# Kernel tuning notes

Measured on AMD Instinct MI355X. Metric: run time of the kernel, lower is better.

Reference implementation:

```python
import jax, jax.numpy as jnp
import numpy as np

N_NODES = 50000
N_EDGES = 800000
IN_FEATS = 128
HIDDEN = 128
NUM_CLASSES = 47


def setup_inputs() -> dict:
    key = jax.random.key(0)
    k1, k2, k3, k4 = jax.random.split(key, 4)
    features = jax.random.normal(k1, (N_NODES, IN_FEATS), dtype=jnp.float32)
    edge_index = jax.random.randint(k2, (2, N_EDGES), 0, N_NODES, dtype=jnp.int32)
    # Glorot-style init for weights, zeros for bias (DGL GraphConv defaults)
    W1 = jax.random.normal(k3, (IN_FEATS, HIDDEN), dtype=jnp.float32) * (1.0 / np.sqrt(IN_FEATS))
    b1 = jnp.zeros((HIDDEN,), dtype=jnp.float32)
    W2 = jax.random.normal(k4, (HIDDEN, NUM_CLASSES), dtype=jnp.float32) * (1.0 / np.sqrt(HIDDEN))
    b2 = jnp.zeros((NUM_CLASSES,), dtype=jnp.float32)
    return {"features": features, "edge_index": edge_index,
            "W1": W1, "b1": b1, "W2": W2, "b2": b2}


def _graph_conv(x, W, b, src, dst, norm_src, norm_dst, n_nodes):
    # DGL GraphConv, norm='both': D_dst^{-1/2} A D_src^{-1/2} (X W) + b
    h = (x * norm_src[:, None]) @ W            # transform before aggregation
    agg = jax.ops.segment_sum(h[src], dst, num_segments=n_nodes)
    return agg * norm_dst[:, None] + b


def reference(features, edge_index, W1, b1, W2, b2):
    src, dst = edge_index[0], edge_index[1]
    n = features.shape[0]
    ones = jnp.ones((src.shape[0],), dtype=features.dtype)
    deg_out = jax.ops.segment_sum(ones, src, num_segments=n)
    deg_in = jax.ops.segment_sum(ones, dst, num_segments=n)
    norm_src = jax.lax.rsqrt(jnp.clip(deg_out, 1.0))   # d_out^{-1/2}, clamp >= 1
    norm_dst = jax.lax.rsqrt(jnp.clip(deg_in, 1.0))    # d_in^{-1/2}, clamp >= 1

    h = _graph_conv(features, W1, b1, src, dst, norm_src, norm_dst, n)
    h = jax.nn.relu(h)
    out = _graph_conv(h, W2, b2, src, dst, norm_src, norm_dst, n)
    return out
```

## Files before the change

kernel.cpp:

```cpp
#include <hip/hip_runtime.h>
#include <hip/hip_fp16.h>

#define N_NODES 50000
#define N_EDGES 800000
#define IN_F 128
#define HID 128
#define NCLS 47
#define H2S 48
#define W2C 64
#define NCH 196
#define NB 128
#define CHUNK 6250
#define PDW 12500
#define HHALF 6250
#define FQ 3125
#define NHIST 512
#define G1ROWS 256
#define G2ROWS 128


typedef _Float16 f16x8 __attribute__((ext_vector_type(8)));
typedef float f32x4 __attribute__((ext_vector_type(4)));

struct __align__(8)  h2x2 { __half2 a, b; };
struct __align__(16) h2x4 { __half2 a, b, c, d; };

__global__ __launch_bounds__(512) void hist_kernel(const int* __restrict__ ei,
                                                   unsigned int* __restrict__ Pdst,
                                                   unsigned int* __restrict__ Psrc,
                                                   const float* __restrict__ W1,
                                                   const float* __restrict__ W2,
                                                   __half* __restrict__ W1Th,
                                                   __half* __restrict__ W1Tl,
                                                   __half* __restrict__ W2Th,
                                                   __half* __restrict__ W2Tl) {
    __shared__ unsigned int h[HHALF];
    const int t = threadIdx.x;
    const int job = blockIdx.x;
    if (job >= NHIST) {
        if (job == NHIST) {
            for (int i2 = t; i2 < W2C * HID; i2 += 512) {
                int cc = i2 >> 7, k = i2 & 127;
                float w = (cc < NCLS) ? W2[k * NCLS + cc] : 0.f;
                __half hv = __float2half_rn(w);
                W2Th[i2] = hv;
                W2Tl[i2] = __float2half_rn(w - __half2float(hv));
            }
        } else {
            for (int i2 = t; i2 < IN_F * HID; i2 += 512) {
                int cc = i2 >> 7, k = i2 & 127;
                float w = W1[k * HID + cc];
                __half hv = __float2half_rn(w);
                W1Th[i2] = hv;
                W1Tl[i2] = __float2half_rn(w - __half2float(hv));
            }
        }
        return;
    }
    const bool is_src = job >= NHIST / 2;
    const int half = (job >> 7) & 1;
    const int chunk = job & (NB - 1);
    const int* ids = is_src ? ei : ei + N_EDGES;
    uint2* h2 = (uint2*)h;
    for (int j = t; j < HHALF / 2; j += 512) h2[j] = make_uint2(0u, 0u);
    __syncthreads();
    const int e0 = chunk * CHUNK;
    const int lo = half * HHALF;
    const int2* e2p = (const int2*)(ids + e0);
    for (int k = t; k < CHUNK / 2; k += 512) {
        int2 v2 = e2p[k];
        int r0 = (v2.x >> 2) - lo;
        if ((unsigned)r0 < HHALF) atomicAdd(&h[r0], 1u << ((v2.x & 3) * 8));
        int r1 = (v2.y >> 2) - lo;
        if ((unsigned)r1 < HHALF) atomicAdd(&h[r1], 1u << ((v2.y & 3) * 8));
    }
    __syncthreads();
    unsigned int* P = (is_src ? Psrc : Pdst) + (size_t)chunk * PDW + lo;
    uint2* P2 = (uint2*)P;
    for (int j = t; j < HHALF / 2; j += 512) P2[j] = h2[j];
}

__global__ __launch_bounds__(256) void reduce_kernel(unsigned int* __restrict__ Pdst,
                                                     const unsigned int* __restrict__ Psrc,
                                                     int* __restrict__ cnt_in,
                                                     float* __restrict__ norm_src,
                                                     float* __restrict__ norm_dst,
                                                     int* __restrict__ chunk_sums) {
    __shared__ int sm[256];
    const int t = threadIdx.x;
    const int j = blockIdx.x * 256 + t;
    int tot = 0;
    if (j < PDW) {
        unsigned int run = 0;
#pragma unroll 8
        for (int b = 0; b < NB; ++b) {
            unsigned int v = Pdst[(size_t)b * PDW + j];
            Pdst[(size_t)b * PDW + j] = run;
            run += v;
        }
        int n0 = run & 0xff, n1 = (run >> 8) & 0xff;
        int n2 = (run >> 16) & 0xff, n3 = (run >> 24) & 0xff;
        *(int4*)&cnt_in[4 * j] = make_int4(n0, n1, n2, n3);
        *(float4*)&norm_dst[4 * j] = make_float4(
            rsqrtf(fmaxf((float)n0, 1.0f)), rsqrtf(fmaxf((float)n1, 1.0f)),
            rsqrtf(fmaxf((float)n2, 1.0f)), rsqrtf(fmaxf((float)n3, 1.0f)));
        tot = n0 + n1 + n2 + n3;
        unsigned int rs = 0;
#pragma unroll 8
        for (int b = 0; b < NB; ++b) rs += Psrc[(size_t)b * PDW + j];
        int s0 = rs & 0xff, s1 = (rs >> 8) & 0xff;
        int s2 = (rs >> 16) & 0xff, s3 = (rs >> 24) & 0xff;
        *(float4*)&norm_src[4 * j] = make_float4(
            rsqrtf(fmaxf((float)s0, 1.0f)), rsqrtf(fmaxf((float)s1, 1.0f)),
            rsqrtf(fmaxf((float)s2, 1.0f)), rsqrtf(fmaxf((float)s3, 1.0f)));
    }
    sm[t] = tot;
    __syncthreads();
    const int g = t & 63;
    for (int off = 32; off > 0; off >>= 1) {
        if (g < off) sm[t] += sm[t + off];
        __syncthreads();
    }
    if (g == 0) chunk_sums[blockIdx.x * 4 + (t >> 6)] = sm[t];
}

__global__ __launch_bounds__(256) void scan3_kernel(const int* __restrict__ cnt_in,
                                                    const int* __restrict__ chunk_sums,
                                                    int* __restrict__ offsets) {
    __shared__ int sm[256];
    const int t = threadIdx.x;
    int v = (t < NCH) ? chunk_sums[t] : 0;
    sm[t] = v;
    __syncthreads();
    for (int off = 1; off < 256; off <<= 1) {
        int u = (t >= off) ? sm[t - off] : 0;
        __syncthreads();
        sm[t] += u;
        __syncthreads();
    }
    const int basev = (blockIdx.x == 0) ? 0 : sm[blockIdx.x - 1];
    __syncthreads();
    const int idx = blockIdx.x * 256 + t;
    int c = (idx < N_NODES) ? cnt_in[idx] : 0;
    sm[t] = c;
    __syncthreads();
    for (int off = 1; off < 256; off <<= 1) {
        int u = (t >= off) ? sm[t - off] : 0;
        __syncthreads();
        sm[t] += u;
        __syncthreads();
    }
    if (idx < N_NODES) offsets[idx] = basev + sm[t] - c;
    if (blockIdx.x == 0 && t == 0) offsets[N_NODES] = N_EDGES;
}

__global__ __launch_bounds__(512) void fill_gemm1_kernel(const int* __restrict__ src,
        const int* __restrict__ dst, const int* __restrict__ offsets,
        const unsigned int* __restrict__ Pdst, int* __restrict__ csr_src,
        const float* __restrict__ X, const __half* __restrict__ W1Th,
        const __half* __restrict__ W1Tl, __half* __restrict__ H1h) {
    __shared__ __align__(16) unsigned int cur[FQ];
    const int t = threadIdx.x;
    if (blockIdx.x < 4 * NB) {
        const int quarter = blockIdx.x >> 7;
        const int chunk = blockIdx.x & (NB - 1);
        for (int j = t; j < FQ; j += 512) cur[j] = 0u;
        __syncthreads();
        const unsigned int* base = Pdst + (size_t)chunk * PDW;
        const int e0 = chunk * CHUNK;
        const int lo = quarter * FQ;
        const int2* d2p = (const int2*)(dst + e0);
        const int2* s2p = (const int2*)(src + e0);
        for (int k = t; k < CHUNK / 2; k += 512) {
            int2 d2 = d2p[k];
            int2 s2 = s2p[k];
            int r0 = (d2.x >> 2) - lo;
            if ((unsigned)r0 < FQ) {
                const int sh = (d2.x & 3) * 8;
                unsigned int old = atomicAdd(&cur[r0], 1u << sh);
                unsigned int rank = (old >> sh) & 0xffu;
                unsigned int bh = (base[d2.x >> 2] >> sh) & 0xffu;
                csr_src[offsets[d2.x] + (int)bh + (int)rank] = s2.x;
            }
            int r1 = (d2.y >> 2) - lo;
            if ((unsigned)r1 < FQ) {
                const int sh = (d2.y & 3) * 8;
                unsigned int old = atomicAdd(&cur[r1], 1u << sh);
                unsigned int rank = (old >> sh) & 0xffu;
                unsigned int bh = (base[d2.y >> 2] >> sh) & 0xffu;
                csr_src[offsets[d2.y] + (int)bh + (int)rank] = s2.y;
            }
        }
    } else {
        const int lane = t & 63;
        const int wv = t >> 6;
        const int r16 = lane & 15;
        const int kg = lane >> 4;
        const int row0 = (blockIdx.x - 4 * NB) * G1ROWS + wv * 32;
        f32x4 acc[2][8] = {};
#pragma unroll
        for (int s = 0; s < 4; ++s) {
            const int k0 = 32 * s + 8 * kg;
            f16x8 ah[2], al[2];
#pragma unroll
            for (int rt = 0; rt < 2; ++rt) {
                int row = row0 + rt * 16 + r16;
                int rc = row < N_NODES ? row : N_NODES - 1;
                const float4 x0 = *(const float4*)&X[(size_t)rc * IN_F + k0];
                const float4 x1 = *(const float4*)&X[(size_t)rc * IN_F + k0 + 4];
                const float xv[8] = {x0.x, x0.y, x0.z, x0.w,
                                     x1.x, x1.y, x1.z, x1.w};
#pragma unroll
                for (int j = 0; j < 8; ++j) {
                    _Float16 hv = (_Float16)xv[j];
                    ah[rt][j] = hv;
                    al[rt][j] = (_Float16)(xv[j] - (float)hv);
                }
            }
#pragma unroll
            for (int tt = 0; tt < 8; ++tt) {
                const f16x8 bh = *(const f16x8*)&W1Th[(16 * tt + r16) * IN_F + k0];
                const f16x8 bl = *(const f16x8*)&W1Tl[(16 * tt + r16) * IN_F + k0];
#pragma unroll
                for (int rt = 0; rt < 2; ++rt) {
                    acc[rt][tt] = __builtin_amdgcn_mfma_f32_16x16x32_f16(
                        ah[rt], bh, acc[rt][tt], 0, 0, 0);
                    acc[rt][tt] = __builtin_amdgcn_mfma_f32_16x16x32_f16(
                        al[rt], bh, acc[rt][tt], 0, 0, 0);
                    acc[rt][tt] = __builtin_amdgcn_mfma_f32_16x16x32_f16(
                        ah[rt], bl, acc[rt][tt], 0, 0, 0);
                }
            }
        }
#pragma unroll
        for (int rt = 0; rt < 2; ++rt)
#pragma unroll
            for (int j = 0; j < 4; ++j) {
                const int row = row0 + rt * 16 + 4 * kg + j;
                if (row < N_NODES) {
#pragma unroll
                    for (int tt = 0; tt < 8; ++tt)
                        H1h[(size_t)row * HID + 16 * tt + r16] =
                            __float2half_rn(acc[rt][tt][j]);
                }
            }
    }
}

__global__ __launch_bounds__(256) void gather1_kernel(const __half* __restrict__ H1h,
        const int* __restrict__ offsets, const int* __restrict__ csr_src,
        const float* __restrict__ b1, const float* __restrict__ norm_src,
        const float* __restrict__ norm_dst, __half* __restrict__ Hrelu16) {
    const int lane = threadIdx.x & 63;
    const int q = lane >> 4;
    const int fl = lane & 15;
    const int row = blockIdx.x * 4 + (threadIdx.x >> 6);
    const int beg = offsets[row], end = offsets[row + 1];
    float a0 = 0.f, a1 = 0.f, a2 = 0.f, a3 = 0.f;
    float a4 = 0.f, a5 = 0.f, a6 = 0.f, a7 = 0.f;
    for (int base = beg; base < end; base += 64) {
        int idx = 0;
        float nsv = 0.f;
        if (base + lane < end) {
            idx = csr_src[base + lane];
            nsv = norm_src[idx];
        }
        const int cnt = min(end - base, 64);
        for (int j = 0; j < cnt; j += 16) {
            int e0 = j + q, e1 = j + 4 + q, e2 = j + 8 + q, e3 = j + 12 + q;
            int s0 = __shfl(idx, e0);  float n0 = __shfl(nsv, e0);
            int s1 = __shfl(idx, e1);  float n1 = __shfl(nsv, e1);
            int s2 = __shfl(idx, e2);  float n2 = __shfl(nsv, e2);
            int s3 = __shfl(idx, e3);  float n3 = __shfl(nsv, e3);
            h2x4 v0 = *(const h2x4*)&H1h[(size_t)s0 * HID + 8 * fl];
            h2x4 v1 = *(const h2x4*)&H1h[(size_t)s1 * HID + 8 * fl];
            h2x4 v2 = *(const h2x4*)&H1h[(size_t)s2 * HID + 8 * fl];
            h2x4 v3 = *(const h2x4*)&H1h[(size_t)s3 * HID + 8 * fl];
            float2 f;
            f = __half22float2(v0.a); a0 = fmaf(f.x, n0, a0); a1 = fmaf(f.y, n0, a1);
            f = __half22float2(v0.b); a2 = fmaf(f.x, n0, a2); a3 = fmaf(f.y, n0, a3);
            f = __half22float2(v0.c); a4 = fmaf(f.x, n0, a4); a5 = fmaf(f.y, n0, a5);
            f = __half22float2(v0.d); a6 = fmaf(f.x, n0, a6); a7 = fmaf(f.y, n0, a7);
            f = __half22float2(v1.a); a0 = fmaf(f.x, n1, a0); a1 = fmaf(f.y, n1, a1);
            f = __half22float2(v1.b); a2 = fmaf(f.x, n1, a2); a3 = fmaf(f.y, n1, a3);
            f = __half22float2(v1.c); a4 = fmaf(f.x, n1, a4); a5 = fmaf(f.y, n1, a5);
            f = __half22float2(v1.d); a6 = fmaf(f.x, n1, a6); a7 = fmaf(f.y, n1, a7);
            f = __half22float2(v2.a); a0 = fmaf(f.x, n2, a0); a1 = fmaf(f.y, n2, a1);
            f = __half22float2(v2.b); a2 = fmaf(f.x, n2, a2); a3 = fmaf(f.y, n2, a3);
            f = __half22float2(v2.c); a4 = fmaf(f.x, n2, a4); a5 = fmaf(f.y, n2, a5);
            f = __half22float2(v2.d); a6 = fmaf(f.x, n2, a6); a7 = fmaf(f.y, n2, a7);
            f = __half22float2(v3.a); a0 = fmaf(f.x, n3, a0); a1 = fmaf(f.y, n3, a1);
            f = __half22float2(v3.b); a2 = fmaf(f.x, n3, a2); a3 = fmaf(f.y, n3, a3);
            f = __half22float2(v3.c); a4 = fmaf(f.x, n3, a4); a5 = fmaf(f.y, n3, a5);
            f = __half22float2(v3.d); a6 = fmaf(f.x, n3, a6); a7 = fmaf(f.y, n3, a7);
        }
    }
    a0 += __shfl_xor(a0, 16); a1 += __shfl_xor(a1, 16);
    a2 += __shfl_xor(a2, 16); a3 += __shfl_xor(a3, 16);
    a4 += __shfl_xor(a4, 16); a5 += __shfl_xor(a5, 16);
    a6 += __shfl_xor(a6, 16); a7 += __shfl_xor(a7, 16);
    a0 += __shfl_xor(a0, 32); a1 += __shfl_xor(a1, 32);
    a2 += __shfl_xor(a2, 32); a3 += __shfl_xor(a3, 32);
    a4 += __shfl_xor(a4, 32); a5 += __shfl_xor(a5, 32);
    a6 += __shfl_xor(a6, 32); a7 += __shfl_xor(a7, 32);
    if (lane < 16) {
        float nd = norm_dst[row], ns = norm_src[row];
        float4 bA = *(const float4*)&b1[8 * fl];
        float4 bB = *(const float4*)&b1[8 * fl + 4];
        float o0 = fmaxf(fmaf(a0, nd, bA.x), 0.f) * ns;
        float o1 = fmaxf(fmaf(a1, nd, bA.y), 0.f) * ns;
        float o2 = fmaxf(fmaf(a2, nd, bA.z), 0.f) * ns;
        float o3 = fmaxf(fmaf(a3, nd, bA.w), 0.f) * ns;
        float o4 = fmaxf(fmaf(a4, nd, bB.x), 0.f) * ns;
        float o5 = fmaxf(fmaf(a5, nd, bB.y), 0.f) * ns;
        float o6 = fmaxf(fmaf(a6, nd, bB.z), 0.f) * ns;
        float o7 = fmaxf(fmaf(a7, nd, bB.w), 0.f) * ns;
        h2x4 p = {__floats2half2_rn(o0, o1), __floats2half2_rn(o2, o3),
                  __floats2half2_rn(o4, o5), __floats2half2_rn(o6, o7)};
        *(h2x4*)&Hrelu16[(size_t)row * HID + 8 * fl] = p;
    }
}

__global__ __launch_bounds__(256) void gemm2_kernel(const __half* __restrict__ Hrelu16,
                                                    const __half* __restrict__ W2Th,
                                                    const __half* __restrict__ W2Tl,
                                                    __half* __restrict__ H2h) {
    const int lane = threadIdx.x & 63;
    const int wv = threadIdx.x >> 6;
    const int r16 = lane & 15;
    const int kg = lane >> 4;
    const int row0 = blockIdx.x * G2ROWS + wv * 32;
    f32x4 acc[2][3] = {};
#pragma unroll
    for (int s = 0; s < 4; ++s) {
        const int k0 = 32 * s + 8 * kg;
        f16x8 a[2];
#pragma unroll
        for (int rt = 0; rt < 2; ++rt) {
            int row = row0 + rt * 16 + r16;
            int rc = row < N_NODES ? row : N_NODES - 1;
            a[rt] = *(const f16x8*)&Hrelu16[(size_t)rc * HID + k0];
        }
#pragma unroll
        for (int tt = 0; tt < 3; ++tt) {
            const f16x8 bh = *(const f16x8*)&W2Th[(16 * tt + r16) * HID + k0];
            const f16x8 bl = *(const f16x8*)&W2Tl[(16 * tt + r16) * HID + k0];
#pragma unroll
            for (int rt = 0; rt < 2; ++rt) {
                acc[rt][tt] = __builtin_amdgcn_mfma_f32_16x16x32_f16(
                    a[rt], bh, acc[rt][tt], 0, 0, 0);
                acc[rt][tt] = __builtin_amdgcn_mfma_f32_16x16x32_f16(
                    a[rt], bl, acc[rt][tt], 0, 0, 0);
            }
        }
    }
#pragma unroll
    for (int rt = 0; rt < 2; ++rt)
#pragma unroll
        for (int j = 0; j < 4; ++j) {
            const int row = row0 + rt * 16 + 4 * kg + j;
            if (row < N_NODES) {
#pragma unroll
                for (int tt = 0; tt < 3; ++tt)
                    H2h[(size_t)row * H2S + 16 * tt + r16] =
                        __float2half_rn(acc[rt][tt][j]);
            }
        }
}

__global__ __launch_bounds__(256) void gather2_kernel(const __half* __restrict__ H2h,
        const int* __restrict__ offsets, const int* __restrict__ csr_src,
        const float* __restrict__ b2, const float* __restrict__ norm_dst,
        float* __restrict__ out) {
    const int lane = threadIdx.x & 63;
    const int row = blockIdx.x * 4 + (threadIdx.x >> 6);
    const int beg = offsets[row], end = offsets[row + 1];
    const int cl = min(lane, H2S - 1);
    float acc = 0.f;
    for (int base = beg; base < end; base += 64) {
        int idx = 0;
        float wv = 0.f;
        if (base + lane < end) {
            idx = csr_src[base + lane];
            wv = 1.f;
        }
        const int cnt = min(end - base, 64);
        for (int j = 0; j < cnt; j += 4) {
            int s0 = __shfl(idx, j);     float w0 = __shfl(wv, j);
            int s1 = __shfl(idx, j + 1); float w1 = __shfl(wv, j + 1);
            int s2 = __shfl(idx, j + 2); float w2 = __shfl(wv, j + 2);
            int s3 = __shfl(idx, j + 3); float w3 = __shfl(wv, j + 3);
            float f0 = __half2float(H2h[(size_t)s0 * H2S + cl]);
            float f1 = __half2float(H2h[(size_t)s1 * H2S + cl]);
            float f2 = __half2float(H2h[(size_t)s2 * H2S + cl]);
            float f3 = __half2float(H2h[(size_t)s3 * H2S + cl]);
            acc = fmaf(f0, w0, acc);
            acc = fmaf(f1, w1, acc);
            acc = fmaf(f2, w2, acc);
            acc = fmaf(f3, w3, acc);
        }
    }
    if (lane < NCLS) out[(size_t)row * NCLS + lane] = acc * norm_dst[row] + b2[lane];
}

extern "C" void kernel_launch(void* const* d_in, const int* in_sizes, int n_in,
                              void* d_out, int out_size, void* d_ws, size_t ws_size,
                              hipStream_t stream) {
    const float* X  = (const float*)d_in[0];
    const int*   ei = (const int*)d_in[1];
    const float* W1 = (const float*)d_in[2];
    const float* b1 = (const float*)d_in[3];
    const float* W2 = (const float*)d_in[4];
    const float* b2 = (const float*)d_in[5];
    float* out = (float*)d_out;

    const int* src = ei;
    const int* dst = ei + N_EDGES;

    char* w = (char*)d_ws;
    auto alloc = [&](size_t bytes) {
        char* p = w;
        w += (bytes + 255) & ~(size_t)255;
        return p;
    };
    float*  norm_src   = (float*)alloc(N_NODES * 4);
    float*  norm_dst   = (float*)alloc(N_NODES * 4);
    int*    cnt_in     = (int*)alloc(N_NODES * 4);
    int*    offsets    = (int*)alloc((N_NODES + 1) * 4);
    int*    csr_src    = (int*)alloc((size_t)N_EDGES * 4);
    int*    chunk_sums = (int*)alloc(NCH * 4);
    __half* W1Th       = (__half*)alloc((size_t)IN_F * HID * 2);
    __half* W1Tl       = (__half*)alloc((size_t)IN_F * HID * 2);
    __half* W2Th       = (__half*)alloc((size_t)W2C * HID * 2);
    __half* W2Tl       = (__half*)alloc((size_t)W2C * HID * 2);
    __half* H1h        = (__half*)alloc((size_t)N_NODES * HID * 2);
    __half* Hrelu16    = (__half*)alloc((size_t)N_NODES * HID * 2);
    __half* H2h        = (__half*)alloc((size_t)N_NODES * H2S * 2);
    unsigned int* Pdst = (unsigned int*)alloc((size_t)NB * PDW * 4);
    unsigned int* Psrc = (unsigned int*)alloc((size_t)NB * PDW * 4);

    const int g1_blocks = (N_NODES + G1ROWS - 1) / G1ROWS;
    const int g2_blocks = (N_NODES + G2ROWS - 1) / G2ROWS;
    hist_kernel<<<NHIST + 2, 512, 0, stream>>>(ei, Pdst, Psrc, W1, W2,
                                               W1Th, W1Tl, W2Th, W2Tl);
    reduce_kernel<<<(PDW + 255) / 256, 256, 0, stream>>>(Pdst, Psrc, cnt_in,
                                                         norm_src, norm_dst, chunk_sums);
    scan3_kernel<<<NCH, 256, 0, stream>>>(cnt_in, chunk_sums, offsets);
    fill_gemm1_kernel<<<4 * NB + g1_blocks, 512, 0, stream>>>(src, dst, offsets,
                                                              Pdst, csr_src,
                                                              X, W1Th, W1Tl, H1h);
    gather1_kernel<<<N_NODES / 4, 256, 0, stream>>>(H1h, offsets, csr_src, b1,
                                                    norm_src, norm_dst, Hrelu16);
    gemm2_kernel<<<g2_blocks, 256, 0, stream>>>(Hrelu16, W2Th, W2Tl, H2h);
    gather2_kernel<<<N_NODES / 4, 256, 0, stream>>>(H2h, offsets, csr_src, b2,
                                                    norm_dst, out);
}
```

Before: 204.0 us.

## Move GEMM1 into histogram kernel and use full-range shared histograms

Weight conversion moves into its own small prep kernel. GEMM1 now runs in the same launch as the degree histogram instead of with the CSR fill. The histogram and fill kernels each keep one full 12500-word shared array per chunk, replacing the half and quarter node-range splits, so each edge chunk is read once. This removes redundant edge reads and lets GEMM1 overlap the histogram phase. The cost is one extra launch, about 50KB of shared memory per block (lower occupancy), and a fill kernel with only 128 blocks, which may underuse the GPU.

```diff
diff --git a/kernel.cpp b/kernel.cpp
--- a/kernel.cpp
+++ b/kernel.cpp
@@ -12,9 +12,6 @@
 #define NB 128
 #define CHUNK 6250
 #define PDW 12500
-#define HHALF 6250
-#define FQ 3125
-#define NHIST 512
 #define G1ROWS 256
 #define G2ROWS 128
 
@@ -25,59 +22,112 @@
 struct __align__(8)  h2x2 { __half2 a, b; };
 struct __align__(16) h2x4 { __half2 a, b, c, d; };
 
-__global__ __launch_bounds__(512) void hist_kernel(const int* __restrict__ ei,
-                                                   unsigned int* __restrict__ Pdst,
-                                                   unsigned int* __restrict__ Psrc,
-                                                   const float* __restrict__ W1,
+__global__ __launch_bounds__(256) void prep_kernel(const float* __restrict__ W1,
                                                    const float* __restrict__ W2,
                                                    __half* __restrict__ W1Th,
                                                    __half* __restrict__ W1Tl,
                                                    __half* __restrict__ W2Th,
                                                    __half* __restrict__ W2Tl) {
-    __shared__ unsigned int h[HHALF];
+    const int b = blockIdx.x, t = threadIdx.x;
+    if (b < 32) {
+        const int i0 = b * 512;
+        for (int i2 = i0 + t; i2 < i0 + 512; i2 += 256) {
+            int cc = i2 >> 7, k = i2 & 127;
+            float w = W1[k * HID + cc];
+            __half hv = __float2half_rn(w);
+            W1Th[i2] = hv;
+            W1Tl[i2] = __float2half_rn(w - __half2float(hv));
+        }
+    } else {
+        const int i0 = (b - 32) * 512;
+        for (int i2 = i0 + t; i2 < i0 + 512; i2 += 256) {
+            int cc = i2 >> 7, k = i2 & 127;
+            float w = (cc < NCLS) ? W2[k * NCLS + cc] : 0.f;
+            __half hv = __float2half_rn(w);
+            W2Th[i2] = hv;
+            W2Tl[i2] = __float2half_rn(w - __half2float(hv));
+        }
+    }
+}
+
+__global__ __launch_bounds__(512) void hist_gemm1_kernel(const int* __restrict__ ei,
+        unsigned int* __restrict__ Pdst, unsigned int* __restrict__ Psrc,
+        const float* __restrict__ X, const __half* __restrict__ W1Th,
+        const __half* __restrict__ W1Tl, __half* __restrict__ H1h) {
+    __shared__ unsigned int h[PDW];
     const int t = threadIdx.x;
-    const int job = blockIdx.x;
-    if (job >= NHIST) {
-        if (job == NHIST) {
-            for (int i2 = t; i2 < W2C * HID; i2 += 512) {
-                int cc = i2 >> 7, k = i2 & 127;
-                float w = (cc < NCLS) ? W2[k * NCLS + cc] : 0.f;
-                __half hv = __float2half_rn(w);
-                W2Th[i2] = hv;
-                W2Tl[i2] = __float2half_rn(w - __half2float(hv));
+    if (blockIdx.x < 2 * NB) {
+        const bool is_src = blockIdx.x >= NB;
+        const int chunk = blockIdx.x & (NB - 1);
+        const int* ids = is_src ? ei : ei + N_EDGES;
+        uint2* h2 = (uint2*)h;
+        for (int j = t; j < PDW / 2; j += 512) h2[j] = make_uint2(0u, 0u);
+        __syncthreads();
+        const int e0 = chunk * CHUNK;
+        const int2* e2p = (const int2*)(ids + e0);
+        for (int k = t; k < CHUNK / 2; k += 512) {
+            int2 v2 = e2p[k];
+            atomicAdd(&h[v2.x >> 2], 1u << ((v2.x & 3) * 8));
+            atomicAdd(&h[v2.y >> 2], 1u << ((v2.y & 3) * 8));
+        }
+        __syncthreads();
+        unsigned int* P = (is_src ? Psrc : Pdst) + (size_t)chunk * PDW;
+        uint2* P2 = (uint2*)P;
+        for (int j = t; j < PDW / 2; j += 512) P2[j] = h2[j];
+    } else {
+        const int lane = t & 63;
+        const int wv = t >> 6;
+        const int r16 = lane & 15;
+        const int kg = lane >> 4;
+        const int row0 = (blockIdx.x - 2 * NB) * G1ROWS + wv * 32;
+        f32x4 acc[2][8] = {};
+#pragma unroll
+        for (int s = 0; s < 4; ++s) {
+            const int k0 = 32 * s + 8 * kg;
+            f16x8 ah[2], al[2];
+#pragma unroll
+            for (int rt = 0; rt < 2; ++rt) {
+                int row = row0 + rt * 16 + r16;
+                int rc = row < N_NODES ? row : N_NODES - 1;
+                const float4 x0 = *(const float4*)&X[(size_t)rc * IN_F + k0];
+                const float4 x1 = *(const float4*)&X[(size_t)rc * IN_F + k0 + 4];
+                const float xv[8] = {x0.x, x0.y, x0.z, x0.w,
+                                     x1.x, x1.y, x1.z, x1.w};
+#pragma unroll
+                for (int j = 0; j < 8; ++j) {
+                    _Float16 hv = (_Float16)xv[j];
+                    ah[rt][j] = hv;
+                    al[rt][j] = (_Float16)(xv[j] - (float)hv);
+                }
             }
-        } else {
-            for (int i2 = t; i2 < IN_F * HID; i2 += 512) {
-                int cc = i2 >> 7, k = i2 & 127;
-                float w = W1[k * HID + cc];
-                __half hv = __float2half_rn(w);
-                W1Th[i2] = hv;
-                W1Tl[i2] = __float2half_rn(w - __half2float(hv));
+#pragma unroll
+            for (int tt = 0; tt < 8; ++tt) {
+                const f16x8 bh = *(const f16x8*)&W1Th[(16 * tt + r16) * IN_F + k0];
+                const f16x8 bl = *(const f16x8*)&W1Tl[(16 * tt + r16) * IN_F + k0];
+#pragma unroll
+                for (int rt = 0; rt < 2; ++rt) {
+                    acc[rt][tt] = __builtin_amdgcn_mfma_f32_16x16x32_f16(
+                        ah[rt], bh, acc[rt][tt], 0, 0, 0);
+                    acc[rt][tt] = __builtin_amdgcn_mfma_f32_16x16x32_f16(
+                        al[rt], bh, acc[rt][tt], 0, 0, 0);
+                    acc[rt][tt] = __builtin_amdgcn_mfma_f32_16x16x32_f16(
+                        ah[rt], bl, acc[rt][tt], 0, 0, 0);
+                }
             }
         }
-        return;
-    }
-    const bool is_src = job >= NHIST / 2;
-    const int half = (job >> 7) & 1;
-    const int chunk = job & (NB - 1);
-    const int* ids = is_src ? ei : ei + N_EDGES;
-    uint2* h2 = (uint2*)h;
-    for (int j = t; j < HHALF / 2; j += 512) h2[j] = make_uint2(0u, 0u);
-    __syncthreads();
-    const int e0 = chunk * CHUNK;
-    const int lo = half * HHALF;
-    const int2* e2p = (const int2*)(ids + e0);
-    for (int k = t; k < CHUNK / 2; k += 512) {
-        int2 v2 = e2p[k];
-        int r0 = (v2.x >> 2) - lo;
-        if ((unsigned)r0 < HHALF) atomicAdd(&h[r0], 1u << ((v2.x & 3) * 8));
-        int r1 = (v2.y >> 2) - lo;
-        if ((unsigned)r1 < HHALF) atomicAdd(&h[r1], 1u << ((v2.y & 3) * 8));
-    }
-    __syncthreads();
-    unsigned int* P = (is_src ? Psrc : Pdst) + (size_t)chunk * PDW + lo;
-    uint2* P2 = (uint2*)P;
-    for (int j = t; j < HHALF / 2; j += 512) P2[j] = h2[j];
+#pragma unroll
+        for (int rt = 0; rt < 2; ++rt)
+#pragma unroll
+            for (int j = 0; j < 4; ++j) {
+                const int row = row0 + rt * 16 + 4 * kg + j;
+                if (row < N_NODES) {
+#pragma unroll
+                    for (int tt = 0; tt < 8; ++tt)
+                        H1h[(size_t)row * HID + 16 * tt + r16] =
+                            __float2half_rn(acc[rt][tt][j]);
+                }
+            }
+    }
 }
 
 __global__ __launch_bounds__(256) void reduce_kernel(unsigned int* __restrict__ Pdst,
@@ -154,96 +204,38 @@
     if (blockIdx.x == 0 && t == 0) offsets[N_NODES] = N_EDGES;
 }
 
-__global__ __launch_bounds__(512) void fill_gemm1_kernel(const int* __restrict__ src,
+__global__ __launch_bounds__(512) void fill_kernel(const int* __restrict__ src,
         const int* __restrict__ dst, const int* __restrict__ offsets,
-        const unsigned int* __restrict__ Pdst, int* __restrict__ csr_src,
-        const float* __restrict__ X, const __half* __restrict__ W1Th,
-        const __half* __restrict__ W1Tl, __half* __restrict__ H1h) {
-    __shared__ __align__(16) unsigned int cur[FQ];
+        const unsigned int* __restrict__ Pdst, int* __restrict__ csr_src) {
+    __shared__ __align__(16) unsigned int cur[PDW];
     const int t = threadIdx.x;
-    if (blockIdx.x < 4 * NB) {
-        const int quarter = blockIdx.x >> 7;
-        const int chunk = blockIdx.x & (NB - 1);
-        for (int j = t; j < FQ; j += 512) cur[j] = 0u;
-        __syncthreads();
-        const unsigned int* base = Pdst + (size_t)chunk * PDW;
-        const int e0 = chunk * CHUNK;
-        const int lo = quarter * FQ;
-        const int2* d2p = (const int2*)(dst + e0);
-        const int2* s2p = (const int2*)(src + e0);
-        for (int k = t; k < CHUNK / 2; k += 512) {
-            int2 d2 = d2p[k];
-            int2 s2 = s2p[k];
-            int r0 = (d2.x >> 2) - lo;
-            if ((unsigned)r0 < FQ) {
-                const int sh = (d2.x & 3) * 8;
-                unsigned int old = atomicAdd(&cur[r0], 1u << sh);
-                unsigned int rank = (old >> sh) & 0xffu;
-                unsigned int bh = (base[d2.x >> 2] >> sh) & 0xffu;
-                csr_src[offsets[d2.x] + (int)bh + (int)rank] = s2.x;
-            }
-            int r1 = (d2.y >> 2) - lo;
-            if ((unsigned)r1 < FQ) {
-                const int sh = (d2.y & 3) * 8;
-                unsigned int old = atomicAdd(&cur[r1], 1u << sh);
-                unsigned int rank = (old >> sh) & 0xffu;
-                unsigned int bh = (base[d2.y >> 2] >> sh) & 0xffu;
-                csr_src[offsets[d2.y] + (int)bh + (int)rank] = s2.y;
-            }
-        }
-    } else {
-        const int lane = t & 63;
-        const int wv = t >> 6;
-        const int r16 = lane & 15;
-        const int kg = lane >> 4;
-        const int row0 = (blockIdx.x - 4 * NB) * G1ROWS + wv * 32;
-        f32x4 acc[2][8] = {};
-#pragma unroll
-        for (int s = 0; s < 4; ++s) {
-            const int k0 = 32 * s + 8 * kg;
-            f16x8 ah[2], al[2];
-#pragma unroll
-            for (int rt = 0; rt < 2; ++rt) {
-                int row = row0 + rt * 16 + r16;
-                int rc = row < N_NODES ? row : N_NODES - 1;
-                const float4 x0 = *(const float4*)&X[(size_t)rc * IN_F + k0];
-                const float4 x1 = *(const float4*)&X[(size_t)rc * IN_F + k0 + 4];
-                const float xv[8] = {x0.x, x0.y, x0.z, x0.w,
-                                     x1.x, x1.y, x1.z, x1.w};
-#pragma unroll
-                for (int j = 0; j < 8; ++j) {
-                    _Float16 hv = (_Float16)xv[j];
-                    ah[rt][j] = hv;
-                    al[rt][j] = (_Float16)(xv[j] - (float)hv);
-                }
-            }
-#pragma unroll
-            for (int tt = 0; tt < 8; ++tt) {
-                const f16x8 bh = *(const f16x8*)&W1Th[(16 * tt + r16) * IN_F + k0];
-                const f16x8 bl = *(const f16x8*)&W1Tl[(16 * tt + r16) * IN_F + k0];
-#pragma unroll
-                for (int rt = 0; rt < 2; ++rt) {
-                    acc[rt][tt] = __builtin_amdgcn_mfma_f32_16x16x32_f16(
-                        ah[rt], bh, acc[rt][tt], 0, 0, 0);
-                    acc[rt][tt] = __builtin_amdgcn_mfma_f32_16x16x32_f16(
-                        al[rt], bh, acc[rt][tt], 0, 0, 0);
-                    acc[rt][tt] = __builtin_amdgcn_mfma_f32_16x16x32_f16(
-                        ah[rt], bl, acc[rt][tt], 0, 0, 0);
-                }
-            }
-        }
-#pragma unroll
-        for (int rt = 0; rt < 2; ++rt)
-#pragma unroll
-            for (int j = 0; j < 4; ++j) {
-                const int row = row0 + rt * 16 + 4 * kg + j;
-                if (row < N_NODES) {
-#pragma unroll
-                    for (int tt = 0; tt < 8; ++tt)
-                        H1h[(size_t)row * HID + 16 * tt + r16] =
-                            __float2half_rn(acc[rt][tt][j]);
-                }
-            }
+    const int chunk = blockIdx.x;
+    uint2* c2 = (uint2*)cur;
+    for (int j = t; j < PDW / 2; j += 512) c2[j] = make_uint2(0u, 0u);
+    __syncthreads();
+    const unsigned int* base = Pdst + (size_t)chunk * PDW;
+    const int e0 = chunk * CHUNK;
+    const int2* d2p = (const int2*)(dst + e0);
+    const int2* s2p = (const int2*)(src + e0);
+    for (int k = t; k < CHUNK / 2; k += 512) {
+        int2 d2 = d2p[k];
+        int2 s2 = s2p[k];
+        {
+            const int d = d2.x;
+            const int sh = (d & 3) * 8;
+            const unsigned int bw = base[d >> 2];
+            const int off = offsets[d];
+            unsigned int old = atomicAdd(&cur[d >> 2], 1u << sh);
+            csr_src[off + (int)((bw >> sh) & 0xffu) + (int)((old >> sh) & 0xffu)] = s2.x;
+        }
+        {
+            const int d = d2.y;
+            const int sh = (d & 3) * 8;
+            const unsigned int bw = base[d >> 2];
+            const int off = offsets[d];
+            unsigned int old = atomicAdd(&cur[d >> 2], 1u << sh);
+            csr_src[off + (int)((bw >> sh) & 0xffu) + (int)((old >> sh) & 0xffu)] = s2.y;
+        }
     }
 }
 
@@ -441,14 +433,13 @@
 
     const int g1_blocks = (N_NODES + G1ROWS - 1) / G1ROWS;
     const int g2_blocks = (N_NODES + G2ROWS - 1) / G2ROWS;
-    hist_kernel<<<NHIST + 2, 512, 0, stream>>>(ei, Pdst, Psrc, W1, W2,
-                                               W1Th, W1Tl, W2Th, W2Tl);
+    prep_kernel<<<48, 256, 0, stream>>>(W1, W2, W1Th, W1Tl, W2Th, W2Tl);
+    hist_gemm1_kernel<<<2 * NB + g1_blocks, 512, 0, stream>>>(ei, Pdst, Psrc,
+                                                              X, W1Th, W1Tl, H1h);
     reduce_kernel<<<(PDW + 255) / 256, 256, 0, stream>>>(Pdst, Psrc, cnt_in,
                                                          norm_src, norm_dst, chunk_sums);
     scan3_kernel<<<NCH, 256, 0, stream>>>(cnt_in, chunk_sums, offsets);
-    fill_gemm1_kernel<<<4 * NB + g1_blocks, 512, 0, stream>>>(src, dst, offsets,
-                                                              Pdst, csr_src,
-                                                              X, W1Th, W1Tl, H1h);
+    fill_kernel<<<NB, 512, 0, stream>>>(src, dst, offsets, Pdst, csr_src);
     gather1_kernel<<<N_NODES / 4, 256, 0, stream>>>(H1h, offsets, csr_src, b1,
                                                     norm_src, norm_dst, Hrelu16);
     gemm2_kernel<<<g2_blocks, 256, 0, stream>>>(Hrelu16, W2Th, W2Tl, H2h);
```

After: 207.2 us. No clear change (+1.6%).
